# Optimization experiments

Hardware: AMD Instinct MI355X
Metric: run time of the kernel (lower is better)

Reference implementation:

```python
import jax, jax.numpy as jnp
import numpy as np

D = 64        # embedding_size
NU = 200000   # num users
NI = 100000   # num items
E = 1000000   # edges per relation
BN_EPS = 1e-5


def gatv2(h_src, h_dst, src, dst, Wsrc, bsrc, Wdst, bdst, attn, bias, num_dst):
    # DGL GATv2Conv, num_heads=1, negative_slope=0.2, share_weights=False
    fs = h_src @ Wsrc + bsrc                       # [Ns, D]
    fd = h_dst @ Wdst + bdst                       # [Nd, D]
    e = jax.nn.leaky_relu(fs[src] + fd[dst], 0.2) @ attn   # [E]
    m = jax.ops.segment_max(e, dst, num_segments=num_dst)  # edge softmax per dst
    a = jnp.exp(e - m[dst])
    z = jax.ops.segment_sum(a, dst, num_segments=num_dst)
    alpha = a / z[dst]
    out = jax.ops.segment_sum(alpha[:, None] * fs[src], dst, num_segments=num_dst)
    return out + bias


def att_mlp(x, W1, b1, W2, b2, g, be):
    # Linear(2D,2D) -> Linear(2D,1) -> BatchNorm1d(1, training stats) -> LeakyReLU(0.01)
    h = (x @ W1 + b1) @ W2 + b2                    # [N, 1]
    mu = jnp.mean(h)
    var = jnp.mean((h - mu) ** 2)
    h = g * (h - mu) / jnp.sqrt(var + BN_EPS) + be
    return jax.nn.leaky_relu(h, 0.01)


def setup_inputs() -> dict:
    key = jax.random.key(0)
    ks = jax.random.split(key, 48)
    ki = iter(ks)
    rn = lambda shape, s=0.1: jax.random.normal(next(ki), shape, jnp.float32) * s
    inp = {}
    inp["user_emb"] = jax.random.normal(next(ki), (NU, D), jnp.float32)
    inp["item_emb"] = jax.random.normal(next(ki), (NI, D), jnp.float32)
    inp["rate_src"] = jax.random.randint(next(ki), (E,), 0, NU)
    inp["rate_dst"] = jax.random.randint(next(ki), (E,), 0, NI)
    inp["ratedby_src"] = jax.random.randint(next(ki), (E,), 0, NI)
    inp["ratedby_dst"] = jax.random.randint(next(ki), (E,), 0, NU)
    inp["trust_src"] = jax.random.randint(next(ki), (E,), 0, NU)
    inp["trust_dst"] = jax.random.randint(next(ki), (E,), 0, NU)
    for p in ("rate", "rb", "tr"):
        inp[p + "_Wsrc"] = rn((D, D))
        inp[p + "_bsrc"] = rn((D,))
        inp[p + "_Wdst"] = rn((D, D))
        inp[p + "_bdst"] = rn((D,))
        inp[p + "_attn"] = rn((D,))
        inp[p + "_bias"] = rn((D,))
    for p in ("inf", "int"):
        inp[p + "_W1"] = rn((2 * D, 2 * D))
        inp[p + "_b1"] = rn((2 * D,))
        inp[p + "_W2"] = rn((2 * D, 1))
        inp[p + "_b2"] = rn((1,))
        inp[p + "_g"] = jnp.ones((1,), jnp.float32)
        inp[p + "_be"] = jnp.zeros((1,), jnp.float32)
    return inp


def reference(user_emb, item_emb,
              rate_Wsrc, rate_bsrc, rate_Wdst, rate_bdst, rate_attn, rate_bias,
              rb_Wsrc, rb_bsrc, rb_Wdst, rb_bdst, rb_attn, rb_bias,
              tr_Wsrc, tr_bsrc, tr_Wdst, tr_bdst, tr_attn, tr_bias,
              inf_W1, inf_b1, inf_W2, inf_b2, inf_g, inf_be,
              int_W1, int_b1, int_W2, int_b2, int_g, int_be,
              rate_src, rate_dst, ratedby_src, ratedby_dst, trust_src, trust_dst):
    # interest diffusion: user -> item ('rate')
    item_out = gatv2(user_emb, item_emb, rate_src, rate_dst,
                     rate_Wsrc, rate_bsrc, rate_Wdst, rate_bdst,
                     rate_attn, rate_bias, NI) + item_emb
    # interest diffusion: item -> user ('rated-by')
    q_hair = gatv2(item_emb, user_emb, ratedby_src, ratedby_dst,
                   rb_Wsrc, rb_bsrc, rb_Wdst, rb_bdst, rb_attn, rb_bias, NU)
    # influence diffusion: user -> user ('trust')
    p_hair = gatv2(user_emb, user_emb, trust_src, trust_dst,
                   tr_Wsrc, tr_bsrc, tr_Wdst, tr_bdst, tr_attn, tr_bias, NU)
    # attention-gated fusion
    s_inf = att_mlp(jnp.concatenate([user_emb, p_hair], axis=1),
                    inf_W1, inf_b1, inf_W2, inf_b2, inf_g, inf_be)
    s_int = att_mlp(jnp.concatenate([user_emb, q_hair], axis=1),
                    int_W1, int_b1, int_W2, int_b2, int_g, int_be)
    gamma = jax.nn.softmax(jnp.concatenate([s_inf, s_int], axis=1), axis=1)  # [NU, 2]
    user_out = gamma[:, :1] * p_hair + gamma[:, 1:2] * q_hair + user_emb
    return user_out, item_out
```

## Files before the change

kernel.cpp:

```cpp
#include <hip/hip_runtime.h>
#include <cstdint>


#define D 64
#define FH_BLOCKS 1024

__device__ __forceinline__ float waveReduceSum(float v) {
#pragma unroll
  for (int off = 32; off > 0; off >>= 1) v += __shfl_xor(v, off, 64);
  return v;
}

__device__ __forceinline__ void fma4(float4& a, float s, const float4& b) {
  a.x += s * b.x;
  a.y += s * b.y;
  a.z += s * b.z;
  a.w += s * b.w;
}

__global__ __launch_bounds__(256) void proj64_kernel(
    const float* __restrict__ X, const float* __restrict__ W,
    const float* __restrict__ b, float* __restrict__ Y, int N) {
  __shared__ __align__(16) float Ws[64 * 64];
  __shared__ __align__(16) float Xs[64][68];
  const int t = threadIdx.x;
  const int row0 = blockIdx.x * 64;

#pragma unroll
  for (int i = 0; i < 16; ++i) Ws[t + i * 256] = W[t + i * 256];
#pragma unroll
  for (int i = 0; i < 16; ++i) {
    int idx = t + i * 256;
    int r = idx >> 6, k = idx & 63;
    int gr = row0 + r;
    Xs[r][k] = (gr < N) ? X[gr * 64 + k] : 0.f;
  }
  __syncthreads();

  const int jt = (t & 15) * 4;
  const int rt = (t >> 4) * 4;
  float4 a0 = *reinterpret_cast<const float4*>(b + jt);
  float4 a1 = a0, a2 = a0, a3 = a0;

#pragma unroll 4
  for (int k4 = 0; k4 < 16; ++k4) {
    float4 w0 = *reinterpret_cast<const float4*>(&Ws[(k4 * 4 + 0) * 64 + jt]);
    float4 w1 = *reinterpret_cast<const float4*>(&Ws[(k4 * 4 + 1) * 64 + jt]);
    float4 w2 = *reinterpret_cast<const float4*>(&Ws[(k4 * 4 + 2) * 64 + jt]);
    float4 w3 = *reinterpret_cast<const float4*>(&Ws[(k4 * 4 + 3) * 64 + jt]);
    float4 x0 = *reinterpret_cast<const float4*>(&Xs[rt + 0][k4 * 4]);
    float4 x1 = *reinterpret_cast<const float4*>(&Xs[rt + 1][k4 * 4]);
    float4 x2 = *reinterpret_cast<const float4*>(&Xs[rt + 2][k4 * 4]);
    float4 x3 = *reinterpret_cast<const float4*>(&Xs[rt + 3][k4 * 4]);
    fma4(a0, x0.x, w0); fma4(a0, x0.y, w1); fma4(a0, x0.z, w2); fma4(a0, x0.w, w3);
    fma4(a1, x1.x, w0); fma4(a1, x1.y, w1); fma4(a1, x1.z, w2); fma4(a1, x1.w, w3);
    fma4(a2, x2.x, w0); fma4(a2, x2.y, w1); fma4(a2, x2.z, w2); fma4(a2, x2.w, w3);
    fma4(a3, x3.x, w0); fma4(a3, x3.y, w1); fma4(a3, x3.z, w2); fma4(a3, x3.w, w3);
  }

  int gr = row0 + rt;
  if (gr + 0 < N) *reinterpret_cast<float4*>(&Y[(gr + 0) * 64 + jt]) = a0;
  if (gr + 1 < N) *reinterpret_cast<float4*>(&Y[(gr + 1) * 64 + jt]) = a1;
  if (gr + 2 < N) *reinterpret_cast<float4*>(&Y[(gr + 2) * 64 + jt]) = a2;
  if (gr + 3 < N) *reinterpret_cast<float4*>(&Y[(gr + 3) * 64 + jt]) = a3;
}


__global__ __launch_bounds__(256) void hist3_kernel(
    const int* __restrict__ d0, const int* __restrict__ d1,
    const int* __restrict__ d2, int b1, int b2, int* __restrict__ counts,
    int E) {
  int stride = gridDim.x * 256;
  for (int i = blockIdx.x * 256 + threadIdx.x; i < 3 * E; i += stride) {
    int r = (i >= 2 * E) ? 2 : (i >= E ? 1 : 0);
    int j = i - r * E;
    const int* dp = (r == 0) ? d0 : (r == 1) ? d1 : d2;
    int base = (r == 0) ? 0 : (r == 1) ? b1 : b2;
    atomicAdd(&counts[dp[j] + base], 1);
  }
}

__global__ __launch_bounds__(1024) void scan_chunk_kernel(
    const int* __restrict__ counts, int* __restrict__ incl,
    int* __restrict__ chunk_tot, int N) {
  __shared__ int sh[1024];
  int t = threadIdx.x;
  int i = blockIdx.x * 1024 + t;
  int x = (i < N) ? counts[i] : 0;
  sh[t] = x;
  __syncthreads();
#pragma unroll
  for (int off = 1; off < 1024; off <<= 1) {
    int v = (t >= off) ? sh[t - off] : 0;
    __syncthreads();
    sh[t] += v;
    __syncthreads();
  }
  if (i < N) incl[i] = sh[t];
  if (t == 1023) chunk_tot[blockIdx.x] = sh[t];
}

__global__ __launch_bounds__(1024) void scan_tops_kernel(
    const int* __restrict__ chunk_tot, int* __restrict__ chunk_off,
    int nchunks) {
  __shared__ int sh[1024];
  int t = threadIdx.x;
  int x = (t < nchunks) ? chunk_tot[t] : 0;
  sh[t] = x;
  __syncthreads();
#pragma unroll
  for (int off = 1; off < 1024; off <<= 1) {
    int v = (t >= off) ? sh[t - off] : 0;
    __syncthreads();
    sh[t] += v;
    __syncthreads();
  }
  if (t < nchunks) chunk_off[t] = sh[t] - x;
}

__global__ __launch_bounds__(256) void finalize_ptr_kernel(
    const int* __restrict__ incl, const int* __restrict__ chunk_off,
    int* __restrict__ row_ptr, int N) {
  int i = blockIdx.x * 256 + threadIdx.x;
  if (i >= N) return;
  row_ptr[i + 1] = incl[i] + chunk_off[i >> 10];
  if (i == 0) row_ptr[0] = 0;
}

__global__ __launch_bounds__(256) void copy_ptr_kernel(
    const int* __restrict__ row_ptr, int* __restrict__ next, int N) {
  int i = blockIdx.x * 256 + threadIdx.x;
  if (i < N) next[i] = row_ptr[i];
}

__global__ __launch_bounds__(256) void scatter3_kernel(
    const int* __restrict__ s0, const int* __restrict__ d0,
    const int* __restrict__ s1, const int* __restrict__ d1,
    const int* __restrict__ s2, const int* __restrict__ d2, int b1, int b2,
    int* __restrict__ next, int* __restrict__ esrc, int E) {
  int stride = gridDim.x * 256;
  for (int i = blockIdx.x * 256 + threadIdx.x; i < 3 * E; i += stride) {
    int r = (i >= 2 * E) ? 2 : (i >= E ? 1 : 0);
    int j = i - r * E;
    const int* dp = (r == 0) ? d0 : (r == 1) ? d1 : d2;
    const int* sp = (r == 0) ? s0 : (r == 1) ? s1 : s2;
    int base = (r == 0) ? 0 : (r == 1) ? b1 : b2;
    int pos = atomicAdd(&next[dp[j] + base], 1);
    esrc[pos] = sp[j];
  }
}

__global__ __launch_bounds__(256) void gat_row_kernel(
    const float* __restrict__ fs, const float* __restrict__ fd,
    const int* __restrict__ row_ptr, const int* __restrict__ esrc,
    const float* __restrict__ attn, const float* __restrict__ bias,
    const float* __restrict__ resid, float* __restrict__ out, int Nd) {
  const int lane = threadIdx.x & 63;
  const int d = (blockIdx.x * 256 + threadIdx.x) >> 6;
  if (d >= Nd) return;
  const int g = lane >> 4;
  const int c = (lane & 15) * 4;

  const float4 aw = *reinterpret_cast<const float4*>(&attn[c]);
  const float4 fdv = *reinterpret_cast<const float4*>(&fd[d * 64 + c]);
  const int jbeg = row_ptr[d];
  const int jend = row_ptr[d + 1];

  float m = -1e30f, z = 0.f;
  float4 acc = {0.f, 0.f, 0.f, 0.f};
  for (int j = jbeg + g; j < jend; j += 4) {
    int s = esrc[j];
    float4 fsv = *reinterpret_cast<const float4*>(&fs[s * 64 + c]);
    float vx = fsv.x + fdv.x; vx = (vx > 0.f) ? vx : 0.2f * vx;
    float vy = fsv.y + fdv.y; vy = (vy > 0.f) ? vy : 0.2f * vy;
    float vz = fsv.z + fdv.z; vz = (vz > 0.f) ? vz : 0.2f * vz;
    float vw = fsv.w + fdv.w; vw = (vw > 0.f) ? vw : 0.2f * vw;
    float p = vx * aw.x + vy * aw.y + vz * aw.z + vw * aw.w;
#pragma unroll
    for (int off = 1; off < 16; off <<= 1) p += __shfl_xor(p, off, 64);
    float mn = fmaxf(m, p);
    float sc = __expf(m - mn);
    float w = __expf(p - mn);
    z = z * sc + w;
    acc.x = acc.x * sc + w * fsv.x;
    acc.y = acc.y * sc + w * fsv.y;
    acc.z = acc.z * sc + w * fsv.z;
    acc.w = acc.w * sc + w * fsv.w;
    m = mn;
  }
#pragma unroll
  for (int off = 16; off < 64; off <<= 1) {
    float m_o = __shfl_xor(m, off, 64);
    float z_o = __shfl_xor(z, off, 64);
    float ax = __shfl_xor(acc.x, off, 64);
    float ay = __shfl_xor(acc.y, off, 64);
    float az = __shfl_xor(acc.z, off, 64);
    float aww = __shfl_xor(acc.w, off, 64);
    float mn = fmaxf(m, m_o);
    float s0 = __expf(m - mn), s1 = __expf(m_o - mn);
    z = z * s0 + z_o * s1;
    acc.x = acc.x * s0 + ax * s1;
    acc.y = acc.y * s0 + ay * s1;
    acc.z = acc.z * s0 + az * s1;
    acc.w = acc.w * s0 + aww * s1;
    m = mn;
  }
  if (g == 0) {
    float inv = (z > 0.f) ? 1.f / z : 0.f;
    float4 bb = *reinterpret_cast<const float4*>(&bias[c]);
    float4 o;
    o.x = acc.x * inv + bb.x;
    o.y = acc.y * inv + bb.y;
    o.z = acc.z * inv + bb.z;
    o.w = acc.w * inv + bb.w;
    if (resid) {
      float4 rr = *reinterpret_cast<const float4*>(&resid[d * 64 + c]);
      o.x += rr.x; o.y += rr.y; o.z += rr.z; o.w += rr.w;
    }
    *reinterpret_cast<float4*>(&out[d * 64 + c]) = o;
  }
}

__global__ __launch_bounds__(256) void weff_kernel(
    const float* __restrict__ W1i, const float* __restrict__ b1i,
    const float* __restrict__ W2i, const float* __restrict__ b2i,
    const float* __restrict__ W1t, const float* __restrict__ b1t,
    const float* __restrict__ W2t, const float* __restrict__ b2t,
    float* __restrict__ wbuf) {
  int t = threadIdx.x;
  const float* W1 = (t < 128) ? W1i : W1t;
  const float* W2 = (t < 128) ? W2i : W2t;
  int i = t & 127;
  int base = (t < 128) ? 0 : 130;
  float s = 0.f;
  for (int j = 0; j < 128; ++j) s += W1[i * 128 + j] * W2[j];
  wbuf[base + i] = s;
  if (i == 0) {
    const float* b1 = (t < 128) ? b1i : b1t;
    const float* b2 = (t < 128) ? b2i : b2t;
    float c = b2[0];
    for (int j = 0; j < 128; ++j) c += b1[j] * W2[j];
    wbuf[base + 128] = c;
  }
}

__global__ __launch_bounds__(256) void fuse_h_kernel(
    const float* __restrict__ ue, const float* __restrict__ p,
    const float* __restrict__ q, const float* __restrict__ wbuf,
    float* __restrict__ h_inf, float* __restrict__ h_int,
    double* __restrict__ partials, int NU) {
  const int lane = threadIdx.x & 63;
  const int wv = threadIdx.x >> 6;
  const int wave = blockIdx.x * 4 + wv;
  const int nwaves = gridDim.x * 4;

  const float wi_u = wbuf[lane];
  const float wi_p = wbuf[64 + lane];
  const float wt_u = wbuf[130 + lane];
  const float wt_q = wbuf[194 + lane];
  const float ci = wbuf[128];
  const float ct = wbuf[258];

  double s0 = 0., s1 = 0., s2 = 0., s3 = 0.;
  for (int u = wave; u < NU; u += nwaves) {
    float uv = ue[u * 64 + lane];
    float hi = uv * wi_u + p[u * 64 + lane] * wi_p;
    float ht = uv * wt_u + q[u * 64 + lane] * wt_q;
    hi = waveReduceSum(hi) + ci;
    ht = waveReduceSum(ht) + ct;
    if (lane == 0) {
      h_inf[u] = hi;
      h_int[u] = ht;
    }
    s0 += (double)hi;
    s1 += (double)hi * (double)hi;
    s2 += (double)ht;
    s3 += (double)ht * (double)ht;
  }

  __shared__ double sh[4][4];
  if (lane == 0) {
    sh[wv][0] = s0;
    sh[wv][1] = s1;
    sh[wv][2] = s2;
    sh[wv][3] = s3;
  }
  __syncthreads();
  if (threadIdx.x < 4) {
    int k = threadIdx.x;
    partials[blockIdx.x * 4 + k] = sh[0][k] + sh[1][k] + sh[2][k] + sh[3][k];
  }
}

__global__ __launch_bounds__(256) void reduce_stats_kernel(
    const double* __restrict__ partials, double* __restrict__ stats,
    int nblocks) {
  int k = threadIdx.x & 3;
  int bstart = threadIdx.x >> 2;
  double s = 0.;
  for (int b = bstart; b < nblocks; b += 64) s += partials[b * 4 + k];
  __shared__ double sh[256];
  sh[threadIdx.x] = s;
  __syncthreads();
  if (threadIdx.x < 4) {
    double acc = 0.;
    for (int i = 0; i < 64; ++i) acc += sh[i * 4 + threadIdx.x];
    stats[threadIdx.x] = acc;
  }
}

__global__ __launch_bounds__(256) void fuse_out_kernel(
    const float* __restrict__ ue, const float* __restrict__ p,
    const float* __restrict__ q, const float* __restrict__ h_inf,
    const float* __restrict__ h_int, const double* __restrict__ stats,
    const float* __restrict__ gi, const float* __restrict__ bei,
    const float* __restrict__ gt, const float* __restrict__ bet,
    float* __restrict__ out, int NU) {
  int i = blockIdx.x * 256 + threadIdx.x;
  if (i >= NU * 64) return;
  int u = i >> 6;
  double invN = 1.0 / (double)NU;
  float mu_i = (float)(stats[0] * invN);
  float var_i = (float)(stats[1] * invN) - mu_i * mu_i;
  float mu_t = (float)(stats[2] * invN);
  float var_t = (float)(stats[3] * invN) - mu_t * mu_t;
  float si = gi[0] * (h_inf[u] - mu_i) / sqrtf(var_i + 1e-5f) + bei[0];
  si = (si > 0.f) ? si : 0.01f * si;
  float st = gt[0] * (h_int[u] - mu_t) / sqrtf(var_t + 1e-5f) + bet[0];
  st = (st > 0.f) ? st : 0.01f * st;
  float mx = fmaxf(si, st);
  float e0 = expf(si - mx), e1 = expf(st - mx);
  float inv = 1.f / (e0 + e1);
  out[i] = (e0 * inv) * p[i] + (e1 * inv) * q[i] + ue[i];
}

extern "C" void kernel_launch(void* const* d_in, const int* in_sizes, int n_in,
                              void* d_out, int out_size, void* d_ws,
                              size_t ws_size, hipStream_t stream) {
  const float* user_emb = (const float*)d_in[0];
  const float* item_emb = (const float*)d_in[1];
  const int* rate_src = (const int*)d_in[2];
  const int* rate_dst = (const int*)d_in[3];
  const int* rb_src = (const int*)d_in[4];
  const int* rb_dst = (const int*)d_in[5];
  const int* tr_src = (const int*)d_in[6];
  const int* tr_dst = (const int*)d_in[7];
  const float* rate_Wsrc = (const float*)d_in[8];
  const float* rate_bsrc = (const float*)d_in[9];
  const float* rate_Wdst = (const float*)d_in[10];
  const float* rate_bdst = (const float*)d_in[11];
  const float* rate_attn = (const float*)d_in[12];
  const float* rate_bias = (const float*)d_in[13];
  const float* rb_Wsrc = (const float*)d_in[14];
  const float* rb_bsrc = (const float*)d_in[15];
  const float* rb_Wdst = (const float*)d_in[16];
  const float* rb_bdst = (const float*)d_in[17];
  const float* rb_attn = (const float*)d_in[18];
  const float* rb_bias = (const float*)d_in[19];
  const float* tr_Wsrc = (const float*)d_in[20];
  const float* tr_bsrc = (const float*)d_in[21];
  const float* tr_Wdst = (const float*)d_in[22];
  const float* tr_bdst = (const float*)d_in[23];
  const float* tr_attn = (const float*)d_in[24];
  const float* tr_bias = (const float*)d_in[25];
  const float* inf_W1 = (const float*)d_in[26];
  const float* inf_b1 = (const float*)d_in[27];
  const float* inf_W2 = (const float*)d_in[28];
  const float* inf_b2 = (const float*)d_in[29];
  const float* inf_g = (const float*)d_in[30];
  const float* inf_be = (const float*)d_in[31];
  const float* int_W1 = (const float*)d_in[32];
  const float* int_b1 = (const float*)d_in[33];
  const float* int_W2 = (const float*)d_in[34];
  const float* int_b2 = (const float*)d_in[35];
  const float* int_g = (const float*)d_in[36];
  const float* int_be = (const float*)d_in[37];

  const int NU = in_sizes[0] / 64;
  const int NI = in_sizes[1] / 64;
  const int E = in_sizes[2];
  const size_t MX = (size_t)((NU > NI) ? NU : NI);
  const int NT = 2 * NU + NI;

  char* ws = (char*)d_ws;
  size_t off = 0;
  auto alloc = [&](size_t bytes) -> void* {
    void* pp = ws + off;
    off += (bytes + 255) & ~(size_t)255;
    return pp;
  };
  float* fs = (float*)alloc(MX * 64 * 4);
  float* fd = (float*)alloc(MX * 64 * 4);
  float* q_acc = (float*)alloc((size_t)NU * 64 * 4);
  int* cnt = (int*)alloc((size_t)NT * 4);
  int* row_ptr = (int*)alloc(((size_t)NT + 1) * 4);
  int* esrc = (int*)alloc((size_t)3 * E * 4);
  int* chunk_tot = (int*)alloc(1024 * 4);
  int* chunk_off = (int*)alloc(1024 * 4);
  float* h_inf = (float*)alloc((size_t)NU * 4);
  float* h_int = (float*)alloc((size_t)NU * 4);
  float* wbuf = (float*)alloc(272 * 4);
  double* stats = (double*)alloc(4 * 8);
  double* partials = (double*)alloc((size_t)FH_BLOCKS * 4 * 8);

  float* p_acc = (float*)d_out;
  float* item_acc = (float*)d_out + (size_t)NU * 64;

  auto projGrid = [](int n) { return (n + 63) / 64; };
  auto elemGrid = [](int total) { return (total + 255) / 256; };
  const int edgeBlocks = 2048;

  weff_kernel<<<1, 256, 0, stream>>>(inf_W1, inf_b1, inf_W2, inf_b2, int_W1,
                                     int_b1, int_W2, int_b2, wbuf);

  hipMemsetAsync(cnt, 0, (size_t)NT * 4, stream);
  hist3_kernel<<<edgeBlocks, 256, 0, stream>>>(tr_dst, rb_dst, rate_dst, NU,
                                               2 * NU, cnt, E);
  int nchunks = (NT + 1023) / 1024;
  scan_chunk_kernel<<<nchunks, 1024, 0, stream>>>(cnt, cnt, chunk_tot, NT);
  scan_tops_kernel<<<1, 1024, 0, stream>>>(chunk_tot, chunk_off, nchunks);
  finalize_ptr_kernel<<<elemGrid(NT), 256, 0, stream>>>(cnt, chunk_off,
                                                        row_ptr, NT);
  copy_ptr_kernel<<<elemGrid(NT), 256, 0, stream>>>(row_ptr, cnt, NT);
  scatter3_kernel<<<edgeBlocks, 256, 0, stream>>>(
      tr_src, tr_dst, rb_src, rb_dst, rate_src, rate_dst, NU, 2 * NU, cnt,
      esrc, E);

  proj64_kernel<<<projGrid(NU), 256, 0, stream>>>(user_emb, tr_Wsrc, tr_bsrc,
                                                  fs, NU);
  proj64_kernel<<<projGrid(NU), 256, 0, stream>>>(user_emb, tr_Wdst, tr_bdst,
                                                  fd, NU);
  gat_row_kernel<<<(NU + 3) / 4, 256, 0, stream>>>(
      fs, fd, row_ptr, esrc, tr_attn, tr_bias, nullptr, p_acc, NU);

  proj64_kernel<<<projGrid(NI), 256, 0, stream>>>(item_emb, rb_Wsrc, rb_bsrc,
                                                  fs, NI);
  proj64_kernel<<<projGrid(NU), 256, 0, stream>>>(user_emb, rb_Wdst, rb_bdst,
                                                  fd, NU);
  gat_row_kernel<<<(NU + 3) / 4, 256, 0, stream>>>(
      fs, fd, row_ptr + NU, esrc, rb_attn, rb_bias, nullptr, q_acc, NU);

  proj64_kernel<<<projGrid(NU), 256, 0, stream>>>(user_emb, rate_Wsrc,
                                                  rate_bsrc, fs, NU);
  proj64_kernel<<<projGrid(NI), 256, 0, stream>>>(item_emb, rate_Wdst,
                                                  rate_bdst, fd, NI);
  gat_row_kernel<<<(NI + 3) / 4, 256, 0, stream>>>(
      fs, fd, row_ptr + 2 * NU, esrc, rate_attn, rate_bias, item_emb,
      item_acc, NI);

  fuse_h_kernel<<<FH_BLOCKS, 256, 0, stream>>>(user_emb, p_acc, q_acc, wbuf,
                                               h_inf, h_int, partials, NU);
  reduce_stats_kernel<<<1, 256, 0, stream>>>(partials, stats, FH_BLOCKS);
  fuse_out_kernel<<<elemGrid(NU * 64), 256, 0, stream>>>(
      user_emb, p_acc, q_acc, h_inf, h_int, stats, inf_g, inf_be, int_g,
      int_be, (float*)d_out, NU);
}
```

Before: 1.055 ms.

## Build CSR with two-pass bucketed radix partition instead of global atomics

Replaces the global-atomic histogram and scatter for CSR construction with a two-level scheme. Edges are first partitioned into 4096-row buckets using per-block shared-memory histograms and offsets. Per-row counts and the final scatter then use shared-memory atomics within each bucket. The goal is to remove contended random global atomics and scattered writes, at the cost of extra passes and temporary buffers aliased onto fs/fd. NB must stay at or below 256 for the shared histogram.

```diff
diff --git a/kernel.cpp b/kernel.cpp
--- a/kernel.cpp
+++ b/kernel.cpp
@@ -4,6 +4,9 @@
 
 #define D 64
 #define FH_BLOCKS 1024
+#define RPB 4096
+#define RPB_SHIFT 12
+#define NCH 256
 
 __device__ __forceinline__ float waveReduceSum(float v) {
 #pragma unroll
@@ -66,27 +69,52 @@
 }
 
 
-__global__ __launch_bounds__(256) void hist3_kernel(
+__global__ __launch_bounds__(256) void bin_count_kernel(
     const int* __restrict__ d0, const int* __restrict__ d1,
-    const int* __restrict__ d2, int b1, int b2, int* __restrict__ counts,
-    int E) {
-  int stride = gridDim.x * 256;
-  for (int i = blockIdx.x * 256 + threadIdx.x; i < 3 * E; i += stride) {
-    int r = (i >= 2 * E) ? 2 : (i >= E ? 1 : 0);
+    const int* __restrict__ d2, int b1, int b2, int* __restrict__ chunk_hist,
+    int E, int NB, int CH) {
+  __shared__ int hist[256];
+  int t = threadIdx.x;
+  for (int b = t; b < NB; b += 256) hist[b] = 0;
+  __syncthreads();
+  int cstart = blockIdx.x * CH;
+  int cend = min(cstart + CH, 3 * E);
+  for (int i = cstart + t; i < cend; i += 256) {
+    int r = (i >= 2 * E) ? 2 : (i >= E) ? 1 : 0;
     int j = i - r * E;
     const int* dp = (r == 0) ? d0 : (r == 1) ? d1 : d2;
     int base = (r == 0) ? 0 : (r == 1) ? b1 : b2;
-    atomicAdd(&counts[dp[j] + base], 1);
-  }
-}
-
-__global__ __launch_bounds__(1024) void scan_chunk_kernel(
-    const int* __restrict__ counts, int* __restrict__ incl,
-    int* __restrict__ chunk_tot, int N) {
+    int grow = dp[j] + base;
+    atomicAdd(&hist[grow >> RPB_SHIFT], 1);
+  }
+  __syncthreads();
+  for (int b = t; b < NB; b += 256) hist[b] = hist[b];
+  for (int b = t; b < NB; b += 256) chunk_hist[b * NCH + blockIdx.x] = hist[b];
+}
+
+__global__ __launch_bounds__(256) void bin_scan_kernel(
+    int* __restrict__ chunk_hist, int* __restrict__ bucket_tot) {
+  __shared__ int sh[256];
+  int t = threadIdx.x;
+  int x = chunk_hist[blockIdx.x * NCH + t];
+  sh[t] = x;
+  __syncthreads();
+#pragma unroll
+  for (int off = 1; off < 256; off <<= 1) {
+    int v = (t >= off) ? sh[t - off] : 0;
+    __syncthreads();
+    sh[t] += v;
+    __syncthreads();
+  }
+  chunk_hist[blockIdx.x * NCH + t] = sh[t] - x;
+  if (t == 255) bucket_tot[blockIdx.x] = sh[t];
+}
+
+__global__ __launch_bounds__(1024) void scan_tops_kernel(
+    const int* __restrict__ vals, int* __restrict__ out, int n) {
   __shared__ int sh[1024];
   int t = threadIdx.x;
-  int i = blockIdx.x * 1024 + t;
-  int x = (i < N) ? counts[i] : 0;
+  int x = (t < n) ? vals[t] : 0;
   sh[t] = x;
   __syncthreads();
 #pragma unroll
@@ -96,16 +124,60 @@
     sh[t] += v;
     __syncthreads();
   }
-  if (i < N) incl[i] = sh[t];
-  if (t == 1023) chunk_tot[blockIdx.x] = sh[t];
-}
-
-__global__ __launch_bounds__(1024) void scan_tops_kernel(
-    const int* __restrict__ chunk_tot, int* __restrict__ chunk_off,
-    int nchunks) {
+  if (t < n) out[t] = sh[t] - x;
+}
+
+__global__ __launch_bounds__(256) void bin_scatter_kernel(
+    const int* __restrict__ s0, const int* __restrict__ d0,
+    const int* __restrict__ s1, const int* __restrict__ d1,
+    const int* __restrict__ s2, const int* __restrict__ d2, int b1, int b2,
+    const int* __restrict__ chunk_hist, const int* __restrict__ bucket_base,
+    int* __restrict__ bbs, int* __restrict__ bbg, int E, int NB, int CH) {
+  __shared__ int cur[256];
+  int t = threadIdx.x;
+  for (int b = t; b < NB; b += 256)
+    cur[b] = bucket_base[b] + chunk_hist[b * NCH + blockIdx.x];
+  __syncthreads();
+  int cstart = blockIdx.x * CH;
+  int cend = min(cstart + CH, 3 * E);
+  for (int i = cstart + t; i < cend; i += 256) {
+    int r = (i >= 2 * E) ? 2 : (i >= E) ? 1 : 0;
+    int j = i - r * E;
+    const int* dp = (r == 0) ? d0 : (r == 1) ? d1 : d2;
+    const int* sp = (r == 0) ? s0 : (r == 1) ? s1 : s2;
+    int base = (r == 0) ? 0 : (r == 1) ? b1 : b2;
+    int grow = dp[j] + base;
+    int idx = atomicAdd(&cur[grow >> RPB_SHIFT], 1);
+    bbs[idx] = sp[j];
+    bbg[idx] = grow;
+  }
+}
+
+__global__ __launch_bounds__(256) void row_count_kernel(
+    const int* __restrict__ bbg, const int* __restrict__ bucket_base,
+    const int* __restrict__ bucket_tot, int* __restrict__ cnt, int NT) {
+  __shared__ int c4[RPB];
+  int t = threadIdx.x;
+  int b = blockIdx.x;
+  for (int r = t; r < RPB; r += 256) c4[r] = 0;
+  __syncthreads();
+  int ps = bucket_base[b], pe = ps + bucket_tot[b];
+  int row0 = b << RPB_SHIFT;
+  for (int i = ps + t; i < pe; i += 256) atomicAdd(&c4[bbg[i] - row0], 1);
+  __syncthreads();
+  for (int r = t; r < RPB; r += 256) {
+    int row = row0 + r;
+    if (row < NT) cnt[row] = c4[r];
+  }
+}
+
+__global__ __launch_bounds__(1024) void scan_chunk_kernel(
+    const int* __restrict__ counts, int* __restrict__ incl,
+    int* __restrict__ chunk_tot, int N) {
   __shared__ int sh[1024];
   int t = threadIdx.x;
-  int x = (t < nchunks) ? chunk_tot[t] : 0;
+  int i = blockIdx.x * 1024 + t;
+  int x = (i < N) ? counts[i] : 0;
   sh[t] = x;
   __syncthreads();
 #pragma unroll
@@ -115,7 +187,8 @@
     sh[t] += v;
     __syncthreads();
   }
-  if (t < nchunks) chunk_off[t] = sh[t] - x;
+  if (i < N) incl[i] = sh[t];
+  if (t == 1023) chunk_tot[blockIdx.x] = sh[t];
 }
 
 __global__ __launch_bounds__(256) void finalize_ptr_kernel(
@@ -127,26 +200,24 @@
   if (i == 0) row_ptr[0] = 0;
 }
 
-__global__ __launch_bounds__(256) void copy_ptr_kernel(
-    const int* __restrict__ row_ptr, int* __restrict__ next, int N) {
-  int i = blockIdx.x * 256 + threadIdx.x;
-  if (i < N) next[i] = row_ptr[i];
-}
-
-__global__ __launch_bounds__(256) void scatter3_kernel(
-    const int* __restrict__ s0, const int* __restrict__ d0,
-    const int* __restrict__ s1, const int* __restrict__ d1,
-    const int* __restrict__ s2, const int* __restrict__ d2, int b1, int b2,
-    int* __restrict__ next, int* __restrict__ esrc, int E) {
-  int stride = gridDim.x * 256;
-  for (int i = blockIdx.x * 256 + threadIdx.x; i < 3 * E; i += stride) {
-    int r = (i >= 2 * E) ? 2 : (i >= E ? 1 : 0);
-    int j = i - r * E;
-    const int* dp = (r == 0) ? d0 : (r == 1) ? d1 : d2;
-    const int* sp = (r == 0) ? s0 : (r == 1) ? s1 : s2;
-    int base = (r == 0) ? 0 : (r == 1) ? b1 : b2;
-    int pos = atomicAdd(&next[dp[j] + base], 1);
-    esrc[pos] = sp[j];
+__global__ __launch_bounds__(256) void bucket_scatter_kernel(
+    const int* __restrict__ bbs, const int* __restrict__ bbg,
+    const int* __restrict__ bucket_base, const int* __restrict__ bucket_tot,
+    const int* __restrict__ row_ptr, int* __restrict__ esrc, int NT) {
+  __shared__ int cur4[RPB];
+  int t = threadIdx.x;
+  int b = blockIdx.x;
+  int row0 = b << RPB_SHIFT;
+  for (int r = t; r < RPB; r += 256) {
+    int row = row0 + r;
+    if (row < NT) cur4[r] = row_ptr[row];
+  }
+  __syncthreads();
+  int ps = bucket_base[b], pe = ps + bucket_tot[b];
+  for (int i = ps + t; i < pe; i += 256) {
+    int lr = bbg[i] - row0;
+    int pos = atomicAdd(&cur4[lr], 1);
+    esrc[pos] = bbs[i];
   }
 }
 
@@ -381,6 +452,8 @@
   const int E = in_sizes[2];
   const size_t MX = (size_t)((NU > NI) ? NU : NI);
   const int NT = 2 * NU + NI;
+  const int NB = (NT + RPB - 1) >> RPB_SHIFT;
+  const int CH = (3 * E + NCH - 1) / NCH;
 
   char* ws = (char*)d_ws;
   size_t off = 0;
@@ -395,6 +468,9 @@
   int* cnt = (int*)alloc((size_t)NT * 4);
   int* row_ptr = (int*)alloc(((size_t)NT + 1) * 4);
   int* esrc = (int*)alloc((size_t)3 * E * 4);
+  int* chunk_hist = (int*)alloc((size_t)256 * NCH * 4);
+  int* bucket_tot = (int*)alloc(1024 * 4);
+  int* bucket_base = (int*)alloc(1024 * 4);
   int* chunk_tot = (int*)alloc(1024 * 4);
   int* chunk_off = (int*)alloc(1024 * 4);
   float* h_inf = (float*)alloc((size_t)NU * 4);
@@ -403,28 +479,34 @@
   double* stats = (double*)alloc(4 * 8);
   double* partials = (double*)alloc((size_t)FH_BLOCKS * 4 * 8);
 
+  int* bbs = (int*)fs;
+  int* bbg = (int*)fd;
+
   float* p_acc = (float*)d_out;
   float* item_acc = (float*)d_out + (size_t)NU * 64;
 
   auto projGrid = [](int n) { return (n + 63) / 64; };
   auto elemGrid = [](int total) { return (total + 255) / 256; };
-  const int edgeBlocks = 2048;
 
   weff_kernel<<<1, 256, 0, stream>>>(inf_W1, inf_b1, inf_W2, inf_b2, int_W1,
                                      int_b1, int_W2, int_b2, wbuf);
 
-  hipMemsetAsync(cnt, 0, (size_t)NT * 4, stream);
-  hist3_kernel<<<edgeBlocks, 256, 0, stream>>>(tr_dst, rb_dst, rate_dst, NU,
-                                               2 * NU, cnt, E);
+  bin_count_kernel<<<NCH, 256, 0, stream>>>(tr_dst, rb_dst, rate_dst, NU,
+                                            2 * NU, chunk_hist, E, NB, CH);
+  bin_scan_kernel<<<NB, 256, 0, stream>>>(chunk_hist, bucket_tot);
+  scan_tops_kernel<<<1, 1024, 0, stream>>>(bucket_tot, bucket_base, NB);
+  bin_scatter_kernel<<<NCH, 256, 0, stream>>>(
+      tr_src, tr_dst, rb_src, rb_dst, rate_src, rate_dst, NU, 2 * NU,
+      chunk_hist, bucket_base, bbs, bbg, E, NB, CH);
+  row_count_kernel<<<NB, 256, 0, stream>>>(bbg, bucket_base, bucket_tot, cnt,
+                                           NT);
   int nchunks = (NT + 1023) / 1024;
   scan_chunk_kernel<<<nchunks, 1024, 0, stream>>>(cnt, cnt, chunk_tot, NT);
   scan_tops_kernel<<<1, 1024, 0, stream>>>(chunk_tot, chunk_off, nchunks);
   finalize_ptr_kernel<<<elemGrid(NT), 256, 0, stream>>>(cnt, chunk_off,
                                                         row_ptr, NT);
-  copy_ptr_kernel<<<elemGrid(NT), 256, 0, stream>>>(row_ptr, cnt, NT);
-  scatter3_kernel<<<edgeBlocks, 256, 0, stream>>>(
-      tr_src, tr_dst, rb_src, rb_dst, rate_src, rate_dst, NU, 2 * NU, cnt,
-      esrc, E);
+  bucket_scatter_kernel<<<NB, 256, 0, stream>>>(bbs, bbg, bucket_base,
+                                                bucket_tot, row_ptr, esrc, NT);
 
   proj64_kernel<<<projGrid(NU), 256, 0, stream>>>(user_emb, tr_Wsrc, tr_bsrc,
                                                   fs, NU);
```

New measurement: 954.8 us. -9.5%, faster.
